# Performance work log

Measured on AMD Instinct MI355X. Metric: run time of the kernel, lower is better.

## Reference

```python
import jax, jax.numpy as jnp
import numpy as np

D, H, C, T, B = 1024, 128, 256, 16, 8192


def setup_inputs() -> dict:
    key = jax.random.key(0)
    ks = jax.random.split(key, 7)
    s = 0.02
    return {
        "x": jax.random.normal(ks[0], (B, D), dtype=jnp.float32),
        "Wr": jax.random.normal(ks[1], (D, T), dtype=jnp.float32) * s,  # router weight (transposed vs torch)
        "br": jnp.zeros((T,), dtype=jnp.float32),
        "W1": jax.random.normal(ks[2], (T, D, H), dtype=jnp.float32) * s,  # per-task fc1
        "b1": jnp.zeros((T, H), dtype=jnp.float32),
        "W2": jax.random.normal(ks[3], (T, H, C), dtype=jnp.float32) * s,  # per-task fc2
        "b2": jnp.zeros((T, C), dtype=jnp.float32),
    }


def reference(x, Wr, br, W1, b1, W2, b2):
    # Router: softmax over tasks, [B, T]
    task_probs = jax.nn.softmax(x @ Wr + br, axis=1)
    # All task experts as one batched grouped-GEMM pass.
    h = jax.nn.relu(jnp.einsum("bd,tdh->tbh", x, W1) + b1[:, None, :])  # [T, B, H]
    preds = jnp.einsum("tbh,thc->tbc", h, W2) + b2[:, None, :]           # [T, B, C]
    # Weight each task's predictions by its routing probability.
    task_preds = preds * task_probs.T[:, :, None]                         # [T, B, C]
    return task_probs, task_preds
```

## Files before the change

### kernel.cpp

```cpp
#include <hip/hip_runtime.h>

using bf16x8 = __attribute__((ext_vector_type(8))) short;
using f32x4  = __attribute__((ext_vector_type(4))) float;

#define B_SZ 8192
#define D_SZ 1024
#define H_SZ 128
#define C_SZ 256
#define T_SZ 16

__device__ __forceinline__ unsigned short f2bf(float f) {
  unsigned int u = __float_as_uint(f);
  return (unsigned short)((u + 0x7fffu + ((u >> 16) & 1u)) >> 16);
}

__global__ __launch_bounds__(256) void cast_x_kernel(const float* __restrict__ src,
                                                     unsigned short* __restrict__ dst, int n4) {
  int i = blockIdx.x * 256 + threadIdx.x;
  const int stride = gridDim.x * 256;
  for (; i < n4; i += stride) {
    float4 v = ((const float4*)src)[i];
    ushort4 o;
    o.x = f2bf(v.x); o.y = f2bf(v.y); o.z = f2bf(v.z); o.w = f2bf(v.w);
    ((ushort4*)dst)[i] = o;
  }
}

__global__ __launch_bounds__(256) void transpose_cast_kernel(const float* __restrict__ src,
                                                             unsigned short* __restrict__ dst,
                                                             int R, int C, int cshift) {
  __shared__ float tile[32][257];
  const int t = blockIdx.y;
  const int r0 = blockIdx.x * 32;
  const float* s = src + ((size_t)t * R + r0) * C;
  const int n = 32 * C;
  for (int idx = threadIdx.x; idx < n; idx += 256)
    tile[idx >> cshift][idx & (C - 1)] = s[idx];
  __syncthreads();
  unsigned short* d = dst + (size_t)t * C * R + r0;
  for (int idx = threadIdx.x; idx < n; idx += 256) {
    int cc = idx >> 5, rr = idx & 31;
    d[(size_t)cc * R + rr] = f2bf(tile[rr][cc]);
  }
}

__global__ __launch_bounds__(256) void router_kernel(const float* __restrict__ x,
                                                     const float* __restrict__ Wr,
                                                     const float* __restrict__ br,
                                                     float* __restrict__ out0) {
  const int lane = threadIdx.x & 63;
  const int wid  = threadIdx.x >> 6;
  const int brow = blockIdx.x * 16 + wid * 4;
  float acc[4][16];
#pragma unroll
  for (int r = 0; r < 4; ++r)
#pragma unroll
    for (int tt = 0; tt < 16; ++tt) acc[r][tt] = 0.f;

  for (int it = 0; it < 16; ++it) {
    const int d = it * 64 + lane;
    const float4* w4 = (const float4*)(Wr + (size_t)d * 16);
    float4 wa = w4[0], wb = w4[1], wc = w4[2], wd = w4[3];
    const float wv[16] = {wa.x, wa.y, wa.z, wa.w, wb.x, wb.y, wb.z, wb.w,
                          wc.x, wc.y, wc.z, wc.w, wd.x, wd.y, wd.z, wd.w};
#pragma unroll
    for (int r = 0; r < 4; ++r) {
      const float xv = x[(size_t)(brow + r) * 1024 + d];
#pragma unroll
      for (int tt = 0; tt < 16; ++tt) acc[r][tt] += xv * wv[tt];
    }
  }
#pragma unroll
  for (int off = 32; off >= 1; off >>= 1) {
#pragma unroll
    for (int r = 0; r < 4; ++r)
#pragma unroll
      for (int tt = 0; tt < 16; ++tt) acc[r][tt] += __shfl_xor(acc[r][tt], off);
  }
  if (lane == 0) {
#pragma unroll
    for (int r = 0; r < 4; ++r) {
      float v[16]; float m = -1e30f;
#pragma unroll
      for (int tt = 0; tt < 16; ++tt) { v[tt] = acc[r][tt] + br[tt]; m = fmaxf(m, v[tt]); }
      float ssum = 0.f;
#pragma unroll
      for (int tt = 0; tt < 16; ++tt) { v[tt] = __expf(v[tt] - m); ssum += v[tt]; }
      const float inv = 1.0f / ssum;
      float4* o = (float4*)(out0 + (size_t)(brow + r) * 16);
      o[0] = make_float4(v[0] * inv, v[1] * inv, v[2] * inv, v[3] * inv);
      o[1] = make_float4(v[4] * inv, v[5] * inv, v[6] * inv, v[7] * inv);
      o[2] = make_float4(v[8] * inv, v[9] * inv, v[10] * inv, v[11] * inv);
      o[3] = make_float4(v[12] * inv, v[13] * inv, v[14] * inv, v[15] * inv);
    }
  }
}

#define SW_REG 65536

__global__ __launch_bounds__(512, 2) void expert_kernel(
    const unsigned short* __restrict__ xb, const unsigned short* __restrict__ w1b,
    const unsigned short* __restrict__ w2b, const float* __restrict__ b1,
    const float* __restrict__ b2, const float* __restrict__ probs,
    float* __restrict__ out1) {
  __shared__ __align__(16) char smem[98304];
  const int tid  = threadIdx.x;
  const int lane = tid & 63;
  const int w    = tid >> 6;
  const int l16  = lane & 15;
  const int l4   = lane >> 4;

  const int bid = blockIdx.x;
  const int lid = (bid & 7) * 64 + (bid >> 3);
  const int t   = lid & 15;
  const int b0  = (lid >> 4) * 256;

  const unsigned short* gp[6];
  unsigned int ldo[6];
#pragma unroll
  for (int it = 0; it < 6; ++it) {
    if (it < 4) {
      const unsigned int o = (unsigned int)w * 4096u + (unsigned int)it * 1024u + (unsigned int)lane * 16u;
      const int row = (int)(o >> 7);
      const int cb  = (int)((o & 127u) ^ (((unsigned)row & 7u) << 4));
      gp[it]  = xb + (size_t)(b0 + row) * 1024 + (cb >> 1);
      ldo[it] = o;
    } else {
      const unsigned int o = (unsigned int)w * 2048u + (unsigned int)(it - 4) * 1024u + (unsigned int)lane * 16u;
      const int row = (int)(o >> 7);
      const int cb  = (int)((o & 127u) ^ (((unsigned)row & 7u) << 4));
      gp[it]  = w1b + (size_t)(t * 128 + row) * 1024 + (cb >> 1);
      ldo[it] = o;
    }
  }

#define STAGE(curbuf, kt)                                                              \
  {                                                                                    \
    _Pragma("unroll")                                                                  \
    for (int it = 0; it < 6; ++it) {                                                   \
      const unsigned short* g = gp[it] + (kt) * 64;                                    \
      char* dd = smem + (it < 4 ? (curbuf) * 32768 + (int)ldo[it]                      \
                                : SW_REG + (curbuf) * 16384 + (int)ldo[it]);           \
      __builtin_amdgcn_global_load_lds(                                                \
          (const __attribute__((address_space(1))) unsigned int*)g,                    \
          (__attribute__((address_space(3))) unsigned int*)dd, 16, 0, 0);              \
    }                                                                                  \
  }

  const int wn = w & 1;
  const int wm = w >> 1;
  f32x4 acc1[4][4] = {};

#define FC1_COMPUTE(curbuf)                                                            \
  {                                                                                    \
    const int bx_base = (curbuf) * 32768;                                              \
    const int aw_base = SW_REG + (curbuf) * 16384;                                     \
    _Pragma("unroll")                                                                  \
    for (int ks = 0; ks < 2; ++ks) {                                                   \
      const int cb = ks * 64 + l4 * 16;                                                \
      bf16x8 aw[4], bx[4];                                                             \
      _Pragma("unroll")                                                                \
      for (int ni = 0; ni < 4; ++ni) {                                                 \
        const int row = wn * 64 + ni * 16 + l16;                                       \
        aw[ni] = *(const bf16x8*)(smem + aw_base + (row << 7) + (cb ^ ((row & 7) << 4)));\
      }                                                                                \
      _Pragma("unroll")                                                                \
      for (int mi = 0; mi < 4; ++mi) {                                                 \
        const int row = wm * 64 + mi * 16 + l16;                                       \
        bx[mi] = *(const bf16x8*)(smem + bx_base + (row << 7) + (cb ^ ((row & 7) << 4)));\
      }                                                                                \
      _Pragma("unroll")                                                                \
      for (int ni = 0; ni < 4; ++ni)                                                   \
        _Pragma("unroll")                                                              \
        for (int mi = 0; mi < 4; ++mi)                                                 \
          acc1[ni][mi] = __builtin_amdgcn_mfma_f32_16x16x32_bf16(aw[ni], bx[mi], acc1[ni][mi], 0, 0, 0); \
    }                                                                                  \
  }

  STAGE(0, 0);
  __syncthreads();
  int cur = 0;
  for (int kt = 0; kt < 15; ++kt) {
    STAGE(cur ^ 1, kt + 1);
    FC1_COMPUTE(cur);
    __syncthreads();
    cur ^= 1;
  }
  FC1_COMPUTE(cur);
  __syncthreads();

#pragma unroll
  for (int ni = 0; ni < 4; ++ni) {
    const int n0 = wn * 64 + ni * 16 + l4 * 4;
    float bb[4];
#pragma unroll
    for (int r = 0; r < 4; ++r) bb[r] = b1[t * 128 + n0 + r];
#pragma unroll
    for (int mi = 0; mi < 4; ++mi) {
      const int m = wm * 64 + mi * 16 + l16;
      unsigned int pk[2];
#pragma unroll
      for (int h = 0; h < 2; ++h) {
        float v0 = fmaxf(acc1[ni][mi][2 * h + 0] + bb[2 * h + 0], 0.f);
        float v1 = fmaxf(acc1[ni][mi][2 * h + 1] + bb[2 * h + 1], 0.f);
        pk[h] = (unsigned int)f2bf(v0) | ((unsigned int)f2bf(v1) << 16);
      }
      const int byte = (m << 8) + ((n0 * 2) ^ ((m & 7) << 4));
      *(uint2*)(smem + byte) = make_uint2(pk[0], pk[1]);
    }
  }
  __syncthreads();

  const int wm2 = w >> 1;
  const int wc  = w & 1;
  f32x4 acc2[4][8] = {};
  const unsigned short* w2t = w2b + (size_t)t * C_SZ * H_SZ;

#pragma unroll
  for (int ks = 0; ks < 4; ++ks) {
    const int cb = ks * 64 + l4 * 16;
    bf16x8 ah[4];
#pragma unroll
    for (int mi = 0; mi < 4; ++mi) {
      const int row = wm2 * 64 + mi * 16 + l16;
      ah[mi] = *(const bf16x8*)(smem + (row << 8) + (cb ^ ((row & 7) << 4)));
    }
#pragma unroll
    for (int ci = 0; ci < 8; ++ci) {
      const int c = wc * 128 + ci * 16 + l16;
      bf16x8 bw = *(const bf16x8*)(w2t + (size_t)c * 128 + ks * 32 + l4 * 8);
#pragma unroll
      for (int mi = 0; mi < 4; ++mi)
        acc2[mi][ci] = __builtin_amdgcn_mfma_f32_16x16x32_bf16(ah[mi], bw, acc2[mi][ci], 0, 0, 0);
    }
  }

  const size_t outbase = (size_t)t * (size_t)(B_SZ * C_SZ);
#pragma unroll
  for (int mi = 0; mi < 4; ++mi) {
    const int m0 = wm2 * 64 + mi * 16 + l4 * 4;
    float pv[4];
#pragma unroll
    for (int r = 0; r < 4; ++r) pv[r] = probs[(size_t)(b0 + m0 + r) * 16 + t];
#pragma unroll
    for (int ci = 0; ci < 8; ++ci) {
      const int c = wc * 128 + ci * 16 + l16;
      const float bias = b2[t * 256 + c];
#pragma unroll
      for (int r = 0; r < 4; ++r)
        out1[outbase + (size_t)(b0 + m0 + r) * 256 + c] = (acc2[mi][ci][r] + bias) * pv[r];
    }
  }
}

extern "C" void kernel_launch(void* const* d_in, const int* in_sizes, int n_in,
                              void* d_out, int out_size, void* d_ws, size_t ws_size,
                              hipStream_t stream) {
  const float* x  = (const float*)d_in[0];
  const float* Wr = (const float*)d_in[1];
  const float* br = (const float*)d_in[2];
  const float* W1 = (const float*)d_in[3];
  const float* b1 = (const float*)d_in[4];
  const float* W2 = (const float*)d_in[5];
  const float* b2 = (const float*)d_in[6];
  float* out0 = (float*)d_out;
  float* out1 = out0 + (size_t)B_SZ * T_SZ;

  char* ws = (char*)d_ws;
  unsigned short* xb  = (unsigned short*)ws;
  unsigned short* w1b = (unsigned short*)(ws + (size_t)16777216);
  unsigned short* w2b = (unsigned short*)(ws + (size_t)16777216 + 4194304);

  cast_x_kernel<<<2048, 256, 0, stream>>>(x, xb, (B_SZ * D_SZ) / 4);
  transpose_cast_kernel<<<dim3(D_SZ / 32, T_SZ), 256, 0, stream>>>(W1, w1b, D_SZ, H_SZ, 7);
  transpose_cast_kernel<<<dim3(H_SZ / 32, T_SZ), 256, 0, stream>>>(W2, w2b, H_SZ, C_SZ, 8);
  router_kernel<<<B_SZ / 16, 256, 0, stream>>>(x, Wr, br, out0);
  expert_kernel<<<512, 512, 0, stream>>>(xb, w1b, w2b, b1, b2, out0, out1);
}
```

Measured before the change: 109.0 us.

## Fuse x cast into router and rework FC1 pipeline with explicit waitcnt barriers

Folds the fp32-to-bf16 cast of x into the router kernel, so x is read once and one launch disappears. The FC1 loop in the expert kernel is restructured to issue two stages ahead. It uses explicit vmcnt waits, raw s_barrier with sched_barriers, and s_setprio around the MFMA blocks, replacing the __syncthreads pairs. This aims to overlap global-to-LDS loads with compute better, at the cost of hand-tuned wait counts that must match the number of loads per stage.

Result: faster. 104.2 us (-4.4%).

```diff
diff --git a/kernel.cpp b/kernel.cpp
--- a/kernel.cpp
+++ b/kernel.cpp
@@ -9,21 +9,11 @@
 #define C_SZ 256
 #define T_SZ 16
 
+#define SB __builtin_amdgcn_sched_barrier(0)
+
 __device__ __forceinline__ unsigned short f2bf(float f) {
   unsigned int u = __float_as_uint(f);
   return (unsigned short)((u + 0x7fffu + ((u >> 16) & 1u)) >> 16);
-}
-
-__global__ __launch_bounds__(256) void cast_x_kernel(const float* __restrict__ src,
-                                                     unsigned short* __restrict__ dst, int n4) {
-  int i = blockIdx.x * 256 + threadIdx.x;
-  const int stride = gridDim.x * 256;
-  for (; i < n4; i += stride) {
-    float4 v = ((const float4*)src)[i];
-    ushort4 o;
-    o.x = f2bf(v.x); o.y = f2bf(v.y); o.z = f2bf(v.z); o.w = f2bf(v.w);
-    ((ushort4*)dst)[i] = o;
-  }
 }
 
 __global__ __launch_bounds__(256) void transpose_cast_kernel(const float* __restrict__ src,
@@ -44,10 +34,11 @@
   }
 }
 
-__global__ __launch_bounds__(256) void router_kernel(const float* __restrict__ x,
-                                                     const float* __restrict__ Wr,
-                                                     const float* __restrict__ br,
-                                                     float* __restrict__ out0) {
+__global__ __launch_bounds__(256) void router_cast_kernel(const float* __restrict__ x,
+                                                          const float* __restrict__ Wr,
+                                                          const float* __restrict__ br,
+                                                          float* __restrict__ out0,
+                                                          unsigned short* __restrict__ xb) {
   const int lane = threadIdx.x & 63;
   const int wid  = threadIdx.x >> 6;
   const int brow = blockIdx.x * 16 + wid * 4;
@@ -66,6 +57,7 @@
 #pragma unroll
     for (int r = 0; r < 4; ++r) {
       const float xv = x[(size_t)(brow + r) * 1024 + d];
+      xb[(size_t)(brow + r) * 1024 + d] = f2bf(xv);
 #pragma unroll
       for (int tt = 0; tt < 16; ++tt) acc[r][tt] += xv * wv[tt];
     }
@@ -151,43 +143,54 @@
   const int wm = w >> 1;
   f32x4 acc1[4][4] = {};
 
-#define FC1_COMPUTE(curbuf)                                                            \
+#define FC1_PHASE(curbuf, ks)                                                          \
   {                                                                                    \
     const int bx_base = (curbuf) * 32768;                                              \
     const int aw_base = SW_REG + (curbuf) * 16384;                                     \
-    _Pragma("unroll")                                                                  \
-    for (int ks = 0; ks < 2; ++ks) {                                                   \
-      const int cb = ks * 64 + l4 * 16;                                                \
-      bf16x8 aw[4], bx[4];                                                             \
+    const int cb = (ks) * 64 + l4 * 16;                                                \
+    bf16x8 aw[4], bx[4];                                                               \
+    _Pragma("unroll")                                                                  \
+    for (int ni = 0; ni < 4; ++ni) {                                                   \
+      const int row = wn * 64 + ni * 16 + l16;                                         \
+      aw[ni] = *(const bf16x8*)(smem + aw_base + (row << 7) + (cb ^ ((row & 7) << 4)));\
+    }                                                                                  \
+    _Pragma("unroll")                                                                  \
+    for (int mi = 0; mi < 4; ++mi) {                                                   \
+      const int row = wm * 64 + mi * 16 + l16;                                         \
+      bx[mi] = *(const bf16x8*)(smem + bx_base + (row << 7) + (cb ^ ((row & 7) << 4)));\
+    }                                                                                  \
+    __builtin_amdgcn_s_setprio(1);                                                     \
+    _Pragma("unroll")                                                                  \
+    for (int ni = 0; ni < 4; ++ni)                                                     \
       _Pragma("unroll")                                                                \
-      for (int ni = 0; ni < 4; ++ni) {                                                 \
-        const int row = wn * 64 + ni * 16 + l16;                                       \
-        aw[ni] = *(const bf16x8*)(smem + aw_base + (row << 7) + (cb ^ ((row & 7) << 4)));\
-      }                                                                                \
-      _Pragma("unroll")                                                                \
-      for (int mi = 0; mi < 4; ++mi) {                                                 \
-        const int row = wm * 64 + mi * 16 + l16;                                       \
-        bx[mi] = *(const bf16x8*)(smem + bx_base + (row << 7) + (cb ^ ((row & 7) << 4)));\
-      }                                                                                \
-      _Pragma("unroll")                                                                \
-      for (int ni = 0; ni < 4; ++ni)                                                   \
-        _Pragma("unroll")                                                              \
-        for (int mi = 0; mi < 4; ++mi)                                                 \
-          acc1[ni][mi] = __builtin_amdgcn_mfma_f32_16x16x32_bf16(aw[ni], bx[mi], acc1[ni][mi], 0, 0, 0); \
-    }                                                                                  \
+      for (int mi = 0; mi < 4; ++mi)                                                   \
+        acc1[ni][mi] = __builtin_amdgcn_mfma_f32_16x16x32_bf16(aw[ni], bx[mi], acc1[ni][mi], 0, 0, 0); \
+    __builtin_amdgcn_s_setprio(0);                                                     \
   }
 
   STAGE(0, 0);
-  __syncthreads();
-  int cur = 0;
-  for (int kt = 0; kt < 15; ++kt) {
-    STAGE(cur ^ 1, kt + 1);
-    FC1_COMPUTE(cur);
-    __syncthreads();
-    cur ^= 1;
-  }
-  FC1_COMPUTE(cur);
-  __syncthreads();
+  STAGE(1, 1);
+  asm volatile("s_waitcnt vmcnt(6)" ::: "memory");
+  SB; __builtin_amdgcn_s_barrier(); SB;
+
+#pragma unroll
+  for (int kt = 0; kt < 14; ++kt) {
+    const int cur = kt & 1;
+    FC1_PHASE(cur, 0);
+    FC1_PHASE(cur, 1);
+    SB; __builtin_amdgcn_s_barrier(); SB;
+    STAGE(cur, kt + 2);
+    asm volatile("s_waitcnt vmcnt(6)" ::: "memory");
+    SB; __builtin_amdgcn_s_barrier(); SB;
+  }
+  FC1_PHASE(0, 0);
+  FC1_PHASE(0, 1);
+  SB; __builtin_amdgcn_s_barrier(); SB;
+  asm volatile("s_waitcnt vmcnt(0)" ::: "memory");
+  SB; __builtin_amdgcn_s_barrier(); SB;
+  FC1_PHASE(1, 0);
+  FC1_PHASE(1, 1);
+  SB; __builtin_amdgcn_s_barrier(); SB;
 
 #pragma unroll
   for (int ni = 0; ni < 4; ++ni) {
@@ -209,7 +212,8 @@
       *(uint2*)(smem + byte) = make_uint2(pk[0], pk[1]);
     }
   }
-  __syncthreads();
+  asm volatile("s_waitcnt lgkmcnt(0)" ::: "memory");
+  SB; __builtin_amdgcn_s_barrier(); SB;
 
   const int wm2 = w >> 1;
   const int wc  = w & 1;
@@ -271,9 +275,8 @@
   unsigned short* w1b = (unsigned short*)(ws + (size_t)16777216);
   unsigned short* w2b = (unsigned short*)(ws + (size_t)16777216 + 4194304);
 
-  cast_x_kernel<<<2048, 256, 0, stream>>>(x, xb, (B_SZ * D_SZ) / 4);
+  router_cast_kernel<<<B_SZ / 16, 256, 0, stream>>>(x, Wr, br, out0, xb);
   transpose_cast_kernel<<<dim3(D_SZ / 32, T_SZ), 256, 0, stream>>>(W1, w1b, D_SZ, H_SZ, 7);
   transpose_cast_kernel<<<dim3(H_SZ / 32, T_SZ), 256, 0, stream>>>(W2, w2b, H_SZ, C_SZ, 8);
-  router_kernel<<<B_SZ / 16, 256, 0, stream>>>(x, Wr, br, out0);
   expert_kernel<<<512, 512, 0, stream>>>(xb, w1b, w2b, b1, b2, out0, out1);
 }
```
